# Kernel optimization log

Hardware: AMD Instinct MI355X
Metric: run time of the kernel (lower is better)

## Reference

```python
import jax, jax.numpy as jnp
import numpy as np

B, IN, OUT, K, TOPK = 1024, 4096, 4096, 64, 64


def setup_inputs() -> dict:
    key = jax.random.key(0)
    k0, k1, k2, k3 = jax.random.split(key, 4)
    return {
        "x": jax.random.normal(k0, (B, K), dtype=jnp.float32),
        "weight": jax.random.normal(k1, (OUT, IN), dtype=jnp.float32) / np.float32(np.sqrt(IN)),
        "bias": jax.random.normal(k2, (OUT,), dtype=jnp.float32) * 0.01,
        "prev_idx": jax.random.randint(k3, (B, K), 0, IN),
        "top_k": TOPK,
    }


def reference(x, weight, bias, prev_idx, top_k):
    # Per-sample column gather of the weight matrix: (OUT, B, K)
    gathered = jnp.take(weight, prev_idx, axis=1)
    # Batched matvec (torch.bmm with input.unsqueeze(-1)) + bias -> (B, OUT)
    result = jnp.einsum('obk,bk->bo', gathered, x) + bias
    # top-k select; torch.gather(result, 1, topk_indices) == top-k values
    vals, sel = jax.lax.top_k(result, top_k)
    return vals, sel
```

## Files before the change

kernel.cpp:

```cpp
#include <hip/hip_runtime.h>
#include <stdint.h>
#include <math.h>


#define NB    1024
#define NIN   4096
#define NOUT  4096
#define NK    64
#define NTOPK 64

__device__ __forceinline__ int SWZ(int i) { return i ^ ((i >> 3) & 7); }

__global__ __launch_bounds__(256) void pack_kernel(const float* __restrict__ x,
                                                   const int* __restrict__ idx,
                                                   uint4* __restrict__ offs8,
                                                   float4* __restrict__ xs4) {
    int tid = blockIdx.x * 256 + threadIdx.x;
    int b  = tid >> 3;
    int k8 = tid & 7;
    const int4* ip = reinterpret_cast<const int4*>(idx + (b << 6) + (k8 << 3));
    const float4* xp = reinterpret_cast<const float4*>(x + (b << 6) + (k8 << 3));
    int4 ia = ip[0], ib = ip[1];
    float4 xa = xp[0], xb = xp[1];

    unsigned o0 = (unsigned)(SWZ(ia.x) << 4), o1 = (unsigned)(SWZ(ia.y) << 4);
    unsigned o2 = (unsigned)(SWZ(ia.z) << 4), o3 = (unsigned)(SWZ(ia.w) << 4);
    unsigned o4 = (unsigned)(SWZ(ib.x) << 4), o5 = (unsigned)(SWZ(ib.y) << 4);
    unsigned o6 = (unsigned)(SWZ(ib.z) << 4), o7 = (unsigned)(SWZ(ib.w) << 4);

    offs8[(k8 << 10) + b] = make_uint4(o0 | (o1 << 16), o2 | (o3 << 16),
                                       o4 | (o5 << 16), o6 | (o7 << 16));
    xs4[((k8 << 1) + 0) * 1024 + b] = xa;
    xs4[((k8 << 1) + 1) * 1024 + b] = xb;
}

__global__ __launch_bounds__(1024, 8) void gemm_kernel(const uint4* __restrict__ offs8,
                                                       const float4* __restrict__ xs4,
                                                       const float* __restrict__ W,
                                                       const float* __restrict__ bias,
                                                       double* __restrict__ C) {
    __shared__ float4 Wt[NIN];
    const int t  = threadIdx.x;
    const int o0 = blockIdx.x * 4;

    {
        const float4* w0p = reinterpret_cast<const float4*>(W + (size_t)(o0 + 0) * NIN);
        const float4* w1p = reinterpret_cast<const float4*>(W + (size_t)(o0 + 1) * NIN);
        const float4* w2p = reinterpret_cast<const float4*>(W + (size_t)(o0 + 2) * NIN);
        const float4* w3p = reinterpret_cast<const float4*>(W + (size_t)(o0 + 3) * NIN);
        float4 r0 = w0p[t], r1 = w1p[t], r2 = w2p[t], r3 = w3p[t];
        int i0 = t << 2;
        Wt[SWZ(i0 + 0)] = make_float4(r0.x, r1.x, r2.x, r3.x);
        Wt[SWZ(i0 + 1)] = make_float4(r0.y, r1.y, r2.y, r3.y);
        Wt[SWZ(i0 + 2)] = make_float4(r0.z, r1.z, r2.z, r3.z);
        Wt[SWZ(i0 + 3)] = make_float4(r0.w, r1.w, r2.w, r3.w);
    }
    __syncthreads();

    double acc[4];
#pragma unroll
    for (int r = 0; r < 4; ++r) acc[r] = (double)bias[o0 + r];

    const uint4*  op = offs8 + t;
    const float4* xp = xs4 + t;
    const char*   base = reinterpret_cast<const char*>(Wt);

#define CONSUME(WV, XV)                                                       \
    {                                                                         \
        double xd = (double)(XV);                                             \
        acc[0] += xd * (double)(WV).x; acc[1] += xd * (double)(WV).y;         \
        acc[2] += xd * (double)(WV).z; acc[3] += xd * (double)(WV).w;         \
    }

    uint4  o8 = op[0];
    float4 xA = xp[0];
    float4 xB = xp[1024];

#pragma unroll 2
    for (int k8 = 0; k8 < NK / 8; ++k8) {
        int kn = (k8 + 1) & 7;
        uint4  o8n = op[kn << 10];
        float4 xAn = xp[kn << 11];
        float4 xBn = xp[(kn << 11) + 1024];

        float4 w0 = *reinterpret_cast<const float4*>(base + (o8.x & 0xFFFFu));
        float4 w1 = *reinterpret_cast<const float4*>(base + (o8.x >> 16));
        float4 w2 = *reinterpret_cast<const float4*>(base + (o8.y & 0xFFFFu));
        float4 w3 = *reinterpret_cast<const float4*>(base + (o8.y >> 16));
        CONSUME(w0, xA.x)
        CONSUME(w1, xA.y)
        CONSUME(w2, xA.z)
        CONSUME(w3, xA.w)

        float4 w4 = *reinterpret_cast<const float4*>(base + (o8.z & 0xFFFFu));
        float4 w5 = *reinterpret_cast<const float4*>(base + (o8.z >> 16));
        float4 w6 = *reinterpret_cast<const float4*>(base + (o8.w & 0xFFFFu));
        float4 w7 = *reinterpret_cast<const float4*>(base + (o8.w >> 16));
        CONSUME(w4, xB.x)
        CONSUME(w5, xB.y)
        CONSUME(w6, xB.z)
        CONSUME(w7, xB.w)

        o8 = o8n; xA = xAn; xB = xBn;
    }
#undef CONSUME

    double2* dst = reinterpret_cast<double2*>(C + (size_t)t * NOUT + o0);
    dst[0] = make_double2(acc[0], acc[1]);
    dst[1] = make_double2(acc[2], acc[3]);
}

__device__ __forceinline__ unsigned keyf(double d) {
    unsigned u = __float_as_uint((float)d);
    return (u & 0x80000000u) ? ~u : (u | 0x80000000u);
}
__device__ __forceinline__ int HADDR(int bin) { return ((bin & 15) << 8) | (bin >> 4); }

__global__ __launch_bounds__(256) void topk_kernel(const double* __restrict__ C,
                                                   float* __restrict__ outv,
                                                   float* __restrict__ outi) {
    __shared__ unsigned hist[4096];
    __shared__ double   cval[1024];
    __shared__ int      cidx[1024];
    __shared__ unsigned part[256];
    __shared__ int      sBstar;
    __shared__ unsigned sCnt;

    const int t = threadIdx.x;
    const double2* row2 = reinterpret_cast<const double2*>(C + (size_t)blockIdx.x * NOUT);

    double v[16];
#pragma unroll
    for (int q = 0; q < 8; ++q) {
        double2 d = row2[q * 256 + t];
        v[2 * q] = d.x; v[2 * q + 1] = d.y;
    }

    for (int j = t; j < 4096; j += 256) hist[j] = 0u;
    if (t == 0) sCnt = 0u;
    __syncthreads();

#pragma unroll
    for (int q = 0; q < 16; ++q)
        atomicAdd(&hist[HADDR(keyf(v[q]) >> 20)], 1u);
    __syncthreads();

    {
        unsigned s = 0;
#pragma unroll
        for (int q = 0; q < 16; ++q) s += hist[(q << 8) | t];
        part[t] = s;
    }
    __syncthreads();

    if (t < 64) {
        unsigned c0 = part[4 * t + 0], c1 = part[4 * t + 1];
        unsigned c2 = part[4 * t + 2], c3 = part[4 * t + 3];
        unsigned s = c0 + c1 + c2 + c3;
        unsigned suf = s;
        for (int off = 1; off < 64; off <<= 1) {
            unsigned xx = __shfl_down(suf, off);
            if (t + off < 64) suf += xx;
        }
        unsigned below = suf - s;
        part[4 * t + 3] = below + c3;
        part[4 * t + 2] = below + c3 + c2;
        part[4 * t + 1] = below + c3 + c2 + c1;
        part[4 * t + 0] = below + s;
    }
    __syncthreads();

    {
        unsigned run = (t < 255) ? part[t + 1] : 0u;
#pragma unroll
        for (int q = 15; q >= 0; --q) {
            unsigned cge = run + hist[(q << 8) | t];
            if (cge >= 64u && run < 64u) sBstar = t * 16 + q;
            run = cge;
        }
    }
    __syncthreads();

    const unsigned Bstar = (unsigned)sBstar;
#pragma unroll
    for (int q = 0; q < 16; ++q) {
        if ((keyf(v[q]) >> 20) >= Bstar) {
            unsigned pos = atomicAdd(&sCnt, 1u);
            if (pos < 1024u) {
                cval[pos] = v[q];
                cidx[pos] = (q >> 1) * 512 + 2 * t + (q & 1);
            }
        }
    }
    __syncthreads();

    int M = (int)sCnt; if (M > 1024) M = 1024;
    int n = 64; while (n < M) n <<= 1;
    for (int j = M + t; j < n; j += 256) { cval[j] = -INFINITY; cidx[j] = 0x7fffffff; }
    __syncthreads();

    for (int kk = 2; kk <= n; kk <<= 1) {
        for (int jj = kk >> 1; jj > 0; jj >>= 1) {
            for (int i = t; i < n; i += 256) {
                int l = i ^ jj;
                if (l > i) {
                    double v1 = cval[i], v2 = cval[l];
                    int    i1 = cidx[i], i2 = cidx[l];
                    bool first = (v1 > v2) || (v1 == v2 && i1 < i2);
                    bool asc   = ((i & kk) == 0);
                    if (first != asc) {
                        cval[i] = v2; cval[l] = v1;
                        cidx[i] = i2; cidx[l] = i1;
                    }
                }
            }
            __syncthreads();
        }
    }

    if (t < 64) {
        outv[(blockIdx.x << 6) + t] = (float)cval[t];
        outi[(blockIdx.x << 6) + t] = (float)cidx[t];
    }
}

extern "C" void kernel_launch(void* const* d_in, const int* in_sizes, int n_in,
                              void* d_out, int out_size, void* d_ws, size_t ws_size,
                              hipStream_t stream) {
    const float* x    = (const float*)d_in[0];
    const float* W    = (const float*)d_in[1];
    const float* bias = (const float*)d_in[2];
    const int*   idx  = (const int*)d_in[3];

    char*   ws    = (char*)d_ws;
    double* C     = (double*)ws;
    uint4*  offs8 = (uint4*)(ws + (size_t)NB * NOUT * sizeof(double));
    float4* xs4   = (float4*)(ws + (size_t)NB * NOUT * sizeof(double) + 131072);

    float* outv = (float*)d_out;
    float* outi = outv + NB * NTOPK;

    pack_kernel<<<(NB * 8) / 256, 256, 0, stream>>>(x, idx, offs8, xs4);
    gemm_kernel<<<NOUT / 4, 1024, 0, stream>>>(offs8, xs4, W, bias, C);
    topk_kernel<<<NB, 256, 0, stream>>>(C, outv, outi);
}
```

Before: 151.0 us.

## Compute eight output columns per GEMM block using 128KB dynamic LDS

Each GEMM block now stages 8 weight rows into shared memory instead of 4, in two 64KB swizzled halves. Every gathered offset and x value is reused for two float4 weight reads and 8 fp64 accumulators, which halves the per-output index and x loads and the grid size. In exchange, the block needs 128KB of dynamic LDS, which limits each CU to one 1024-thread block. That lowers wave occupancy and leaves less latency hiding for the LDS gathers. The launch bounds hint and a one-time hipFuncSetAttribute call are updated to match.

```diff
diff --git a/kernel.cpp b/kernel.cpp
--- a/kernel.cpp
+++ b/kernel.cpp
@@ -34,42 +34,50 @@
     xs4[((k8 << 1) + 1) * 1024 + b] = xb;
 }
 
-__global__ __launch_bounds__(1024, 8) void gemm_kernel(const uint4* __restrict__ offs8,
+__global__ __launch_bounds__(1024, 4) void gemm_kernel(const uint4* __restrict__ offs8,
                                                        const float4* __restrict__ xs4,
                                                        const float* __restrict__ W,
                                                        const float* __restrict__ bias,
                                                        double* __restrict__ C) {
-    __shared__ float4 Wt[NIN];
+    extern __shared__ float4 Wt[];
     const int t  = threadIdx.x;
-    const int o0 = blockIdx.x * 4;
+    const int o0 = blockIdx.x * 8;
 
     {
-        const float4* w0p = reinterpret_cast<const float4*>(W + (size_t)(o0 + 0) * NIN);
-        const float4* w1p = reinterpret_cast<const float4*>(W + (size_t)(o0 + 1) * NIN);
-        const float4* w2p = reinterpret_cast<const float4*>(W + (size_t)(o0 + 2) * NIN);
-        const float4* w3p = reinterpret_cast<const float4*>(W + (size_t)(o0 + 3) * NIN);
-        float4 r0 = w0p[t], r1 = w1p[t], r2 = w2p[t], r3 = w3p[t];
+        const float4* wp = reinterpret_cast<const float4*>(W) + (size_t)o0 * 1024 + t;
+        float4 r0 = wp[0 * 1024], r1 = wp[1 * 1024], r2 = wp[2 * 1024], r3 = wp[3 * 1024];
+        float4 r4 = wp[4 * 1024], r5 = wp[5 * 1024], r6 = wp[6 * 1024], r7 = wp[7 * 1024];
         int i0 = t << 2;
         Wt[SWZ(i0 + 0)] = make_float4(r0.x, r1.x, r2.x, r3.x);
         Wt[SWZ(i0 + 1)] = make_float4(r0.y, r1.y, r2.y, r3.y);
         Wt[SWZ(i0 + 2)] = make_float4(r0.z, r1.z, r2.z, r3.z);
         Wt[SWZ(i0 + 3)] = make_float4(r0.w, r1.w, r2.w, r3.w);
-    }
-    __syncthreads();
-
-    double acc[4];
-#pragma unroll
-    for (int r = 0; r < 4; ++r) acc[r] = (double)bias[o0 + r];
+        Wt[4096 + SWZ(i0 + 0)] = make_float4(r4.x, r5.x, r6.x, r7.x);
+        Wt[4096 + SWZ(i0 + 1)] = make_float4(r4.y, r5.y, r6.y, r7.y);
+        Wt[4096 + SWZ(i0 + 2)] = make_float4(r4.z, r5.z, r6.z, r7.z);
+        Wt[4096 + SWZ(i0 + 3)] = make_float4(r4.w, r5.w, r6.w, r7.w);
+    }
+    __syncthreads();
+
+    double acc0[4], acc1[4];
+#pragma unroll
+    for (int r = 0; r < 4; ++r) {
+        acc0[r] = (double)bias[o0 + r];
+        acc1[r] = (double)bias[o0 + 4 + r];
+    }
 
     const uint4*  op = offs8 + t;
     const float4* xp = xs4 + t;
-    const char*   base = reinterpret_cast<const char*>(Wt);
-
-#define CONSUME(WV, XV)                                                       \
+    const char*   base0 = reinterpret_cast<const char*>(Wt);
+    const char*   base1 = base0 + 65536;
+
+#define CONSUME2(WA, WB, XV)                                                  \
     {                                                                         \
         double xd = (double)(XV);                                             \
-        acc[0] += xd * (double)(WV).x; acc[1] += xd * (double)(WV).y;         \
-        acc[2] += xd * (double)(WV).z; acc[3] += xd * (double)(WV).w;         \
+        acc0[0] += xd * (double)(WA).x; acc0[1] += xd * (double)(WA).y;       \
+        acc0[2] += xd * (double)(WA).z; acc0[3] += xd * (double)(WA).w;       \
+        acc1[0] += xd * (double)(WB).x; acc1[1] += xd * (double)(WB).y;       \
+        acc1[2] += xd * (double)(WB).z; acc1[3] += xd * (double)(WB).w;       \
     }
 
     uint4  o8 = op[0];
@@ -83,31 +91,52 @@
         float4 xAn = xp[kn << 11];
         float4 xBn = xp[(kn << 11) + 1024];
 
-        float4 w0 = *reinterpret_cast<const float4*>(base + (o8.x & 0xFFFFu));
-        float4 w1 = *reinterpret_cast<const float4*>(base + (o8.x >> 16));
-        float4 w2 = *reinterpret_cast<const float4*>(base + (o8.y & 0xFFFFu));
-        float4 w3 = *reinterpret_cast<const float4*>(base + (o8.y >> 16));
-        CONSUME(w0, xA.x)
-        CONSUME(w1, xA.y)
-        CONSUME(w2, xA.z)
-        CONSUME(w3, xA.w)
-
-        float4 w4 = *reinterpret_cast<const float4*>(base + (o8.z & 0xFFFFu));
-        float4 w5 = *reinterpret_cast<const float4*>(base + (o8.z >> 16));
-        float4 w6 = *reinterpret_cast<const float4*>(base + (o8.w & 0xFFFFu));
-        float4 w7 = *reinterpret_cast<const float4*>(base + (o8.w >> 16));
-        CONSUME(w4, xB.x)
-        CONSUME(w5, xB.y)
-        CONSUME(w6, xB.z)
-        CONSUME(w7, xB.w)
+        {
+            unsigned a0 = o8.x & 0xFFFFu, a1 = o8.x >> 16;
+            float4 w0a = *reinterpret_cast<const float4*>(base0 + a0);
+            float4 w0b = *reinterpret_cast<const float4*>(base1 + a0);
+            float4 w1a = *reinterpret_cast<const float4*>(base0 + a1);
+            float4 w1b = *reinterpret_cast<const float4*>(base1 + a1);
+            CONSUME2(w0a, w0b, xA.x)
+            CONSUME2(w1a, w1b, xA.y)
+        }
+        {
+            unsigned a0 = o8.y & 0xFFFFu, a1 = o8.y >> 16;
+            float4 w0a = *reinterpret_cast<const float4*>(base0 + a0);
+            float4 w0b = *reinterpret_cast<const float4*>(base1 + a0);
+            float4 w1a = *reinterpret_cast<const float4*>(base0 + a1);
+            float4 w1b = *reinterpret_cast<const float4*>(base1 + a1);
+            CONSUME2(w0a, w0b, xA.z)
+            CONSUME2(w1a, w1b, xA.w)
+        }
+        {
+            unsigned a0 = o8.z & 0xFFFFu, a1 = o8.z >> 16;
+            float4 w0a = *reinterpret_cast<const float4*>(base0 + a0);
+            float4 w0b = *reinterpret_cast<const float4*>(base1 + a0);
+            float4 w1a = *reinterpret_cast<const float4*>(base0 + a1);
+            float4 w1b = *reinterpret_cast<const float4*>(base1 + a1);
+            CONSUME2(w0a, w0b, xB.x)
+            CONSUME2(w1a, w1b, xB.y)
+        }
+        {
+            unsigned a0 = o8.w & 0xFFFFu, a1 = o8.w >> 16;
+            float4 w0a = *reinterpret_cast<const float4*>(base0 + a0);
+            float4 w0b = *reinterpret_cast<const float4*>(base1 + a0);
+            float4 w1a = *reinterpret_cast<const float4*>(base0 + a1);
+            float4 w1b = *reinterpret_cast<const float4*>(base1 + a1);
+            CONSUME2(w0a, w0b, xB.z)
+            CONSUME2(w1a, w1b, xB.w)
+        }
 
         o8 = o8n; xA = xAn; xB = xBn;
     }
-#undef CONSUME
+#undef CONSUME2
 
     double2* dst = reinterpret_cast<double2*>(C + (size_t)t * NOUT + o0);
-    dst[0] = make_double2(acc[0], acc[1]);
-    dst[1] = make_double2(acc[2], acc[3]);
+    dst[0] = make_double2(acc0[0], acc0[1]);
+    dst[1] = make_double2(acc0[2], acc0[3]);
+    dst[2] = make_double2(acc1[0], acc1[1]);
+    dst[3] = make_double2(acc1[2], acc1[3]);
 }
 
 __device__ __forceinline__ unsigned keyf(double d) {
@@ -240,7 +269,14 @@
     float* outv = (float*)d_out;
     float* outi = outv + NB * NTOPK;
 
+    static int lds_ok = 0;
+    if (!lds_ok) {
+        hipFuncSetAttribute(reinterpret_cast<const void*>(gemm_kernel),
+                            hipFuncAttributeMaxDynamicSharedMemorySize, 131072);
+        lds_ok = 1;
+    }
+
     pack_kernel<<<(NB * 8) / 256, 256, 0, stream>>>(x, idx, offs8, xs4);
-    gemm_kernel<<<NOUT / 4, 1024, 0, stream>>>(offs8, xs4, W, bias, C);
+    gemm_kernel<<<NOUT / 8, 1024, 131072, stream>>>(offs8, xs4, W, bias, C);
     topk_kernel<<<NB, 256, 0, stream>>>(C, outv, outi);
 }
```

Measured after the change: 153.8 us. Within noise of the previous version (+1.8%).
